# Kernel tuning notes

Measured on AMD Instinct MI355X. Metric: run time of the kernel, lower is better.

Reference implementation:

```python
import jax, jax.numpy as jnp
import numpy as np

VOCAB = 32000
EMB = 512
UNITS = 1024
B, T = 128, 256


def setup_inputs() -> dict:
    key = jax.random.key(0)
    ks = jax.random.split(key, 9)
    s = 0.05
    return {
        "tokens": jax.random.randint(ks[0], (B, T), 0, VOCAB),
        "emb_table": jax.random.normal(ks[1], (VOCAB, EMB), jnp.float32) * s,
        "Wx_f": jax.random.normal(ks[2], (EMB, 3 * UNITS), jnp.float32) * s,
        "Wh_f": jax.random.normal(ks[3], (UNITS, 3 * UNITS), jnp.float32) * s,
        "b_f": jnp.zeros((2, 3 * UNITS), jnp.float32),  # [input_bias, recurrent_bias] (reset_after=True)
        "Wx_b": jax.random.normal(ks[4], (EMB, 3 * UNITS), jnp.float32) * s,
        "Wh_b": jax.random.normal(ks[5], (UNITS, 3 * UNITS), jnp.float32) * s,
        "b_b": jnp.zeros((2, 3 * UNITS), jnp.float32),
        "fc_W": jax.random.normal(ks[6], (2 * UNITS, UNITS), jnp.float32) * s,
        "fc_b": jnp.zeros((UNITS,), jnp.float32),
    }


def _gru_dir(x_proj, mask, Wh, b_rec, reverse):
    # x_proj: [B,T,3U] precomputed input projections (z|r|h gate order, Keras),
    # mask: [B,T] bool. Keras GRU v2 semantics: reset_after=True,
    # sigmoid recurrent activation, tanh activation; masked steps carry state.
    b, u = x_proj.shape[0], Wh.shape[0]

    def step(h, inputs):
        xp, m = inputs  # [B,3U], [B]
        rec = h @ Wh + b_rec  # [B,3U]
        xz, xr, xh = jnp.split(xp, 3, axis=-1)
        rz, rr, rh = jnp.split(rec, 3, axis=-1)
        z = jax.nn.sigmoid(xz + rz)
        r = jax.nn.sigmoid(xr + rr)
        hh = jnp.tanh(xh + r * rh)
        h_new = z * h + (1.0 - z) * hh
        h_new = jnp.where(m[:, None], h_new, h)
        return h_new, h_new

    h0 = jnp.zeros((b, u), x_proj.dtype)
    xs = (jnp.swapaxes(x_proj, 0, 1), jnp.swapaxes(mask, 0, 1))  # time-major
    h_last, outs = jax.lax.scan(step, h0, xs, reverse=reverse)
    return jnp.swapaxes(outs, 0, 1), h_last  # [B,T,U], [B,U]


def reference(tokens, emb_table, Wx_f, Wh_f, b_f, Wx_b, Wh_b, b_b, fc_W, fc_b):
    mask = tokens != 0  # Embedding(mask_zero=True)
    x = emb_table[tokens]  # [B,T,E]
    xp_f = x @ Wx_f + b_f[0]
    xp_b = x @ Wx_b + b_b[0]
    out_f, h_f = _gru_dir(xp_f, mask, Wh_f, b_f[1], reverse=False)
    out_b, h_b = _gru_dir(xp_b, mask, Wh_b, b_b[1], reverse=True)
    output = jnp.concatenate([out_f, out_b], axis=-1)  # [B,T,2U]
    hidden = jnp.concatenate([h_f, h_b], axis=-1) @ fc_W + fc_b  # [B,U]
    return output, hidden
```

## Files before the change

kernel.cpp:

```cpp
#include <hip/hip_runtime.h>


#define T_SEQ 256
#define BATCH 128
#define EMB_D 512
#define UNITS 1024
#define NROWS (BATCH * T_SEQ)
#define N3U 3072
#define N6U 6144

typedef __attribute__((ext_vector_type(8))) __bf16 bfv8;
typedef __attribute__((ext_vector_type(4))) float f32x4;

__device__ inline unsigned short f2bf(float f) {
  union { float f; unsigned int u; } x; x.f = f;
  unsigned int u = x.u;
  unsigned int r = (u + 0x7fffu + ((u >> 16) & 1u)) >> 16;
  return (unsigned short)r;
}
__device__ inline float bf2f(unsigned short h) {
  union { unsigned int u; float f; } x; x.u = ((unsigned int)h) << 16;
  return x.f;
}
__device__ inline f32x4 mfma16(bfv8 a, bfv8 b, f32x4 c) {
  return __builtin_amdgcn_mfma_f32_16x16x32_bf16(a, b, c, 0, 0, 0);
}
__device__ inline void gl_lds16(const unsigned short* g, unsigned short* l) {
  __builtin_amdgcn_global_load_lds(
      (const __attribute__((address_space(1))) void*)g,
      (__attribute__((address_space(3))) void*)l, 16, 0, 0);
}

__global__ __launch_bounds__(256) void k_transpose(const float* __restrict__ src,
                                                   unsigned short* __restrict__ dst,
                                                   int K, int N) {
  __shared__ float tile[32][33];
  int k0 = blockIdx.x * 32, n0 = blockIdx.y * 32;
  int tx = threadIdx.x & 31, ty = threadIdx.x >> 5;
#pragma unroll
  for (int i = 0; i < 4; ++i)
    tile[ty + i * 8][tx] = src[(size_t)(k0 + ty + i * 8) * N + n0 + tx];
  __syncthreads();
#pragma unroll
  for (int i = 0; i < 4; ++i)
    dst[(size_t)(n0 + ty + i * 8) * K + k0 + tx] = f2bf(tile[tx][ty + i * 8]);
}

__global__ __launch_bounds__(256) void k_gather(const int* __restrict__ tokens,
                                                const float* __restrict__ emb,
                                                unsigned short* __restrict__ Xbf) {
  int idx = blockIdx.x * 256 + threadIdx.x;
  int row = idx >> 7;
  int c4 = (idx & 127) * 4;
  int tok = tokens[row];
  float4 v = *(const float4*)(emb + (size_t)tok * EMB_D + c4);
  ushort4 p;
  p.x = f2bf(v.x); p.y = f2bf(v.y); p.z = f2bf(v.z); p.w = f2bf(v.w);
  *(ushort4*)(Xbf + (size_t)row * EMB_D + c4) = p;
}

__global__ __launch_bounds__(256) void k_bias(const float* __restrict__ bf_,
                                              const float* __restrict__ bb_,
                                              float* __restrict__ biasX,
                                              float* __restrict__ biasH) {
  int i = blockIdx.x * 256 + threadIdx.x;
  if (i >= N6U) return;
  if (i < N3U) { biasX[i] = bf_[i];        biasH[i] = bf_[N3U + i]; }
  else         { biasX[i] = bb_[i - N3U];  biasH[i] = bb_[i]; }
}

__global__ __launch_bounds__(256) void k_gemm(const unsigned short* __restrict__ A,
                                              const unsigned short* __restrict__ BT,
                                              const float* __restrict__ bias,
                                              void* __restrict__ C,
                                              int M, int N, int K, int out_f32) {
  __shared__ unsigned short As[128 * 32];
  __shared__ unsigned short Bs[128 * 32];
  const int mt = blockIdx.x, nt = blockIdx.y;
  const int tid = threadIdx.x;
  const int wid = tid >> 6, lane = tid & 63;
  const int wm = (wid >> 1) * 64, wn = (wid & 1) * 64;
  const int l15 = lane & 15, lk = (lane >> 4) * 8;

  f32x4 acc[4][4];
#pragma unroll
  for (int i = 0; i < 4; ++i)
#pragma unroll
    for (int j = 0; j < 4; ++j) acc[i][j] = (f32x4){0.f, 0.f, 0.f, 0.f};

  const int r = tid >> 2;
  const int cc = (tid & 3) * 8;
  const unsigned short* ga0 = A + (size_t)(mt * 128 + r) * K + cc;
  const unsigned short* ga1 = ga0 + (size_t)64 * K;
  const unsigned short* gb0 = BT + (size_t)(nt * 128 + r) * K + cc;
  const unsigned short* gb1 = gb0 + (size_t)64 * K;
  unsigned short* lA0 = As + r * 32 + cc;
  unsigned short* lA1 = As + (64 + r) * 32 + cc;
  unsigned short* lB0 = Bs + r * 32 + cc;
  unsigned short* lB1 = Bs + (64 + r) * 32 + cc;

  for (int k0 = 0; k0 < K; k0 += 32) {
    __syncthreads();
    gl_lds16(ga0 + k0, lA0);
    gl_lds16(ga1 + k0, lA1);
    gl_lds16(gb0 + k0, lB0);
    gl_lds16(gb1 + k0, lB1);
    __syncthreads();
    bfv8 af[4], bfr[4];
#pragma unroll
    for (int i = 0; i < 4; ++i) {
      af[i]  = *(const bfv8*)(As + (wm + i * 16 + l15) * 32 + lk);
      bfr[i] = *(const bfv8*)(Bs + (wn + i * 16 + l15) * 32 + lk);
    }
#pragma unroll
    for (int i = 0; i < 4; ++i)
#pragma unroll
      for (int j = 0; j < 4; ++j) acc[i][j] = mfma16(af[i], bfr[j], acc[i][j]);
  }

#pragma unroll
  for (int j = 0; j < 4; ++j) {
    int col = nt * 128 + wn + j * 16 + l15;
    float bv = bias[col];
#pragma unroll
    for (int i = 0; i < 4; ++i) {
      int row0 = mt * 128 + wm + i * 16 + (lane >> 4) * 4;
#pragma unroll
      for (int q = 0; q < 4; ++q) {
        float v = acc[i][j][q] + bv;
        if (out_f32) ((float*)C)[(size_t)(row0 + q) * N + col] = v;
        else ((unsigned short*)C)[(size_t)(row0 + q) * N + col] = f2bf(v);
      }
    }
  }
}

__global__ __launch_bounds__(256) void k_scan(const unsigned short* __restrict__ XP,
                                              const unsigned short* __restrict__ WhT,
                                              const float* __restrict__ biasH,
                                              const int* __restrict__ tokens,
                                              unsigned short* __restrict__ hb0,
                                              unsigned short* __restrict__ hb1,
                                              float* __restrict__ out,
                                              unsigned int* __restrict__ bar) {
  __shared__ unsigned short Wl[3 * 128 * 16 * 8];
  __shared__ unsigned short bounce[64][16];
  const int bid = blockIdx.x;
  const int dir = bid >> 7;
  const int mg  = (bid >> 6) & 1;
  const int ut  = bid & 63;
  const int u0 = ut * 16, m0 = mg * 64;
  const int grp = bid >> 6;
  const int sub = bid & 7;

  for (int c = threadIdx.x; c < 6144; c += 256) {
    const int g  = c >> 11;
    const int kb = (c >> 4) & 127;
    const int uu = c & 15;
    *(uint4*)(Wl + (((g << 7) | kb) * 16 + uu) * 8) =
        *(const uint4*)(WhT + (((size_t)(dir * N3U + (g << 10) + u0 + uu)) << 10) + (kb << 3));
  }

  const int lane = threadIdx.x & 63, wid = threadIdx.x >> 6;
  const int l15 = lane & 15, hi = lane >> 4;
  const size_t aoff = ((size_t)(m0 + wid * 16 + l15) << 11) + (dir << 10) + (hi << 3);
  const int u = u0 + l15;
  const float bz  = biasH[dir * N3U + u];
  const float brg = biasH[dir * N3U + 1024 + u];
  const float bhg = biasH[dir * N3U + 2048 + u];
  const int ob = m0 + wid * 16 + (hi << 2);
  const int rb = wid * 16 + (hi << 2);
  const size_t woff = (dir << 10) + u;
  const int sr = threadIdx.x >> 2, sc4 = (threadIdx.x & 3) << 2;
  const size_t soff = ((size_t)(m0 + sr) << 11) + (dir << 10) + u0 + sc4;

  float hreg[4] = {0.f, 0.f, 0.f, 0.f};
  __syncthreads();

  for (int s = 0; s < T_SEQ; ++s) {
    const int t = dir ? (T_SEQ - 1 - s) : s;
    const unsigned short* hrd = (s & 1) ? hb0 : hb1;
    unsigned short* hwr       = (s & 1) ? hb1 : hb0;

    float xz[4], xr[4], xh[4]; int tok[4];
#pragma unroll
    for (int q = 0; q < 4; ++q) {
      const size_t xpo = ((size_t)((ob + q) * T_SEQ + t)) * N6U + dir * N3U + u;
      xz[q] = bf2f(XP[xpo]);
      xr[q] = bf2f(XP[xpo + 1024]);
      xh[q] = bf2f(XP[xpo + 2048]);
      tok[q] = tokens[(ob + q) * T_SEQ + t];
    }

    const unsigned short* ap = hrd + aoff;
    f32x4 az0 = {0.f,0.f,0.f,0.f}, az1 = az0, ar0 = az0, ar1 = az0, ah0 = az0, ah1 = az0;
#pragma unroll 4
    for (int ks = 0; ks < 16; ++ks) {
      bfv8 a0 = *(const bfv8*)(ap + (ks << 6));
      bfv8 a1 = *(const bfv8*)(ap + (ks << 6) + 32);
      const unsigned short* wp = Wl + (((ks << 3) + hi) * 16 + l15) * 8;
      bfv8 wz0 = *(const bfv8*)(wp);
      bfv8 wr0 = *(const bfv8*)(wp + (1 << 14));
      bfv8 wh0 = *(const bfv8*)(wp + (2 << 14));
      bfv8 wz1 = *(const bfv8*)(wp + 512);
      bfv8 wr1 = *(const bfv8*)(wp + (1 << 14) + 512);
      bfv8 wh1 = *(const bfv8*)(wp + (2 << 14) + 512);
      az0 = mfma16(a0, wz0, az0); ar0 = mfma16(a0, wr0, ar0); ah0 = mfma16(a0, wh0, ah0);
      az1 = mfma16(a1, wz1, az1); ar1 = mfma16(a1, wr1, ar1); ah1 = mfma16(a1, wh1, ah1);
    }
    f32x4 az = az0 + az1, ar = ar0 + ar1, ah = ah0 + ah1;

#pragma unroll
    for (int q = 0; q < 4; ++q) {
      const float z  = 1.f / (1.f + __expf(-(xz[q] + az[q] + bz)));
      const float r  = 1.f / (1.f + __expf(-(xr[q] + ar[q] + brg)));
      const float hh = tanhf(xh[q] + r * (ah[q] + bhg));
      float hn = z * hreg[q] + (1.f - z) * hh;
      if (tok[q] == 0) hn = hreg[q];
      hreg[q] = hn;
      bounce[rb + q][l15] = f2bf(hn);
      __builtin_nontemporal_store(hn, out + ((size_t)((ob + q) * T_SEQ + t) << 11) + woff);
    }

    __syncthreads();
    {
      unsigned long long v = *(const unsigned long long*)&bounce[sr][sc4];
      __hip_atomic_store((unsigned long long*)(hwr + soff), v,
                         __ATOMIC_RELAXED, __HIP_MEMORY_SCOPE_AGENT);
    }

    if (s + 1 < T_SEQ) {
      __syncthreads();
      if (threadIdx.x == 0)
        __hip_atomic_fetch_add(&bar[((grp << 3) | sub) << 6], 1u,
                               __ATOMIC_RELAXED, __HIP_MEMORY_SCOPE_AGENT);
      if (threadIdx.x < 8) {
        const unsigned tgt = 8u * (unsigned)(s + 1);
        unsigned int* p = &bar[((grp << 3) | (int)threadIdx.x) << 6];
        while (__hip_atomic_load(p, __ATOMIC_RELAXED, __HIP_MEMORY_SCOPE_AGENT) < tgt)
          __builtin_amdgcn_s_sleep(2);
        __builtin_amdgcn_fence(__ATOMIC_ACQUIRE, "agent");
      }
      __syncthreads();
    }
  }
}

extern "C" void kernel_launch(void* const* d_in, const int* in_sizes, int n_in,
                              void* d_out, int out_size, void* d_ws, size_t ws_size,
                              hipStream_t stream) {
  const int* tokens = (const int*)d_in[0];
  const float* emb  = (const float*)d_in[1];
  const float* Wx_f = (const float*)d_in[2];
  const float* Wh_f = (const float*)d_in[3];
  const float* b_f  = (const float*)d_in[4];
  const float* Wx_b = (const float*)d_in[5];
  const float* Wh_b = (const float*)d_in[6];
  const float* b_b  = (const float*)d_in[7];
  const float* fc_W = (const float*)d_in[8];
  const float* fc_b = (const float*)d_in[9];
  float* out = (float*)d_out;

  char* w = (char*)d_ws;
  unsigned short* XP  = (unsigned short*)w; w += (size_t)NROWS * N6U * 2;
  unsigned short* Xbf = (unsigned short*)w; w += (size_t)NROWS * EMB_D * 2;
  unsigned short* WxT = (unsigned short*)w; w += (size_t)N6U * EMB_D * 2;
  unsigned short* WhT = (unsigned short*)w; w += (size_t)N6U * UNITS * 2;
  unsigned short* fcWT = (unsigned short*)w; w += (size_t)UNITS * 2048 * 2;
  unsigned short* hb0 = (unsigned short*)w; w += (size_t)BATCH * 2048 * 2;
  unsigned short* hb1 = (unsigned short*)w; w += (size_t)BATCH * 2048 * 2;
  float* biasX = (float*)w; w += N6U * 4;
  float* biasH = (float*)w; w += N6U * 4;
  unsigned int* bar = (unsigned int*)w; w += 2048 * sizeof(unsigned int);

  (void)hipMemsetAsync((void*)hb0, 0, (size_t)BATCH * 2048 * 2 * 2, stream);
  (void)hipMemsetAsync((void*)bar, 0, 2048 * sizeof(unsigned int), stream);

  k_transpose<<<dim3(EMB_D / 32, N3U / 32), 256, 0, stream>>>(Wx_f, WxT, EMB_D, N3U);
  k_transpose<<<dim3(EMB_D / 32, N3U / 32), 256, 0, stream>>>(Wx_b, WxT + (size_t)N3U * EMB_D, EMB_D, N3U);
  k_transpose<<<dim3(UNITS / 32, N3U / 32), 256, 0, stream>>>(Wh_f, WhT, UNITS, N3U);
  k_transpose<<<dim3(UNITS / 32, N3U / 32), 256, 0, stream>>>(Wh_b, WhT + (size_t)N3U * UNITS, UNITS, N3U);
  k_transpose<<<dim3(2048 / 32, 1024 / 32), 256, 0, stream>>>(fc_W, fcWT, 2048, 1024);
  k_bias<<<24, 256, 0, stream>>>(b_f, b_b, biasX, biasH);
  k_gather<<<(NROWS * 128) / 256, 256, 0, stream>>>(tokens, emb, Xbf);

  k_gemm<<<dim3(NROWS / 128, N6U / 128), 256, 0, stream>>>(Xbf, WxT, biasX, XP, NROWS, N6U, EMB_D, 0);

  k_scan<<<256, 256, 0, stream>>>(XP, WhT, biasH, tokens, hb0, hb1, out, bar);

  k_gemm<<<dim3(1, 8), 256, 0, stream>>>(hb1, fcWT, fc_b, out + (size_t)NROWS * 2048, BATCH, UNITS, 2048, 1);
}
```

Measured before the change: 2.836 ms.

## Retile input projections time-major, prefetch per-step inputs, keep z/r weights in registers

The input-projection GEMM now writes its bf16 output in a time-major, per-block tiled layout, and tokens are transposed to time-major. This lets each scan block fetch a contiguous chunk for the next timestep into registers, overlapping the load with the current step's recurrent matmul, instead of issuing scattered global loads inside the serial loop. The z and r recurrent weight fragments are held in VGPRs, and only the h-gate weights stay in LDS, which cuts LDS traffic per step. The cost is heavy register pressure (64 bfv8 fragments plus prefetch buffers, hence the single-block launch bound) and scattered writes from the GEMM epilogue.

```diff
diff --git a/kernel.cpp b/kernel.cpp
--- a/kernel.cpp
+++ b/kernel.cpp
@@ -8,6 +8,7 @@
 #define NROWS (BATCH * T_SEQ)
 #define N3U 3072
 #define N6U 6144
+#define XT_STRIDE 786432
 
 typedef __attribute__((ext_vector_type(8))) __bf16 bfv8;
 typedef __attribute__((ext_vector_type(4))) float f32x4;
@@ -69,11 +70,18 @@
   else         { biasX[i] = bb_[i - N3U];  biasH[i] = bb_[i]; }
 }
 
+__global__ __launch_bounds__(256) void k_tokt(const int* __restrict__ tokens,
+                                              int* __restrict__ tokT) {
+  int i = blockIdx.x * 256 + threadIdx.x;
+  int b = i >> 8, t = i & 255;
+  tokT[t * BATCH + b] = tokens[i];
+}
+
 __global__ __launch_bounds__(256) void k_gemm(const unsigned short* __restrict__ A,
                                               const unsigned short* __restrict__ BT,
                                               const float* __restrict__ bias,
                                               void* __restrict__ C,
-                                              int M, int N, int K, int out_f32) {
+                                              int M, int N, int K, int mode) {
   __shared__ unsigned short As[128 * 32];
   __shared__ unsigned short Bs[128 * 32];
   const int mt = blockIdx.x, nt = blockIdx.y;
@@ -120,31 +128,45 @@
 
 #pragma unroll
   for (int j = 0; j < 4; ++j) {
-    int col = nt * 128 + wn + j * 16 + l15;
-    float bv = bias[col];
+    const int col = nt * 128 + wn + j * 16 + l15;
+    const float bv = bias[col];
+    const int dirc = (col >= N3U) ? 1 : 0;
+    const int cm = col - dirc * N3U;
+    const int g = cm >> 10;
+    const int uu = cm & 1023;
+    const size_t cbase = (size_t)dirc * 393216 + (size_t)(uu >> 4) * 6144 +
+                         (size_t)g * 16 + (uu & 15);
 #pragma unroll
     for (int i = 0; i < 4; ++i) {
-      int row0 = mt * 128 + wm + i * 16 + (lane >> 4) * 4;
+      const int row0 = mt * 128 + wm + i * 16 + (lane >> 4) * 4;
 #pragma unroll
       for (int q = 0; q < 4; ++q) {
-        float v = acc[i][j][q] + bv;
-        if (out_f32) ((float*)C)[(size_t)(row0 + q) * N + col] = v;
-        else ((unsigned short*)C)[(size_t)(row0 + q) * N + col] = f2bf(v);
+        const float v = acc[i][j][q] + bv;
+        const int row = row0 + q;
+        if (mode == 1) {
+          ((float*)C)[(size_t)row * N + col] = v;
+        } else {
+          const int b = row >> 8, tt = row & 255;
+          ((unsigned short*)C)[(size_t)tt * XT_STRIDE + cbase + (size_t)b * 48] = f2bf(v);
+        }
       }
     }
   }
 }
 
-__global__ __launch_bounds__(256) void k_scan(const unsigned short* __restrict__ XP,
-                                              const unsigned short* __restrict__ WhT,
-                                              const float* __restrict__ biasH,
-                                              const int* __restrict__ tokens,
-                                              unsigned short* __restrict__ hb0,
-                                              unsigned short* __restrict__ hb1,
-                                              float* __restrict__ out,
-                                              unsigned int* __restrict__ bar) {
-  __shared__ unsigned short Wl[3 * 128 * 16 * 8];
-  __shared__ unsigned short bounce[64][16];
+__global__ __launch_bounds__(256, 1) void k_scan(const unsigned short* __restrict__ XPn,
+                                                 const unsigned short* __restrict__ WhT,
+                                                 const float* __restrict__ biasH,
+                                                 const int* __restrict__ tokT,
+                                                 unsigned short* __restrict__ hb0,
+                                                 unsigned short* __restrict__ hb1,
+                                                 float* __restrict__ out,
+                                                 unsigned int* __restrict__ bar) {
+  __shared__ unsigned short Wl[128 * 16 * 8];
+  __shared__ unsigned short xb[64 * 48];
+  __shared__ int tkb[64];
+  __shared__ unsigned short bounce[64 * 24];
+
   const int bid = blockIdx.x;
   const int dir = bid >> 7;
   const int mg  = (bid >> 6) & 1;
@@ -152,27 +174,50 @@
   const int u0 = ut * 16, m0 = mg * 64;
   const int grp = bid >> 6;
   const int sub = bid & 7;
-
-  for (int c = threadIdx.x; c < 6144; c += 256) {
-    const int g  = c >> 11;
-    const int kb = (c >> 4) & 127;
-    const int uu = c & 15;
-    *(uint4*)(Wl + (((g << 7) | kb) * 16 + uu) * 8) =
-        *(const uint4*)(WhT + (((size_t)(dir * N3U + (g << 10) + u0 + uu)) << 10) + (kb << 3));
-  }
-
-  const int lane = threadIdx.x & 63, wid = threadIdx.x >> 6;
+  const int tid = threadIdx.x;
+
+  for (int c = tid; c < 2048; c += 256) {
+    const int kb = c >> 4, uu = c & 15;
+    *(uint4*)(Wl + c * 8) =
+        *(const uint4*)(WhT + (((size_t)(dir * N3U + 2048 + u0 + uu)) << 10) + (kb << 3));
+  }
+
+  const int lane = tid & 63, wid = tid >> 6;
   const int l15 = lane & 15, hi = lane >> 4;
+
+  bfv8 wza[16], wzb[16], wra[16], wrb[16];
+  {
+    const unsigned short* wgz = WhT + (((size_t)(dir * N3U + u0 + l15)) << 10);
+    const unsigned short* wgr = wgz + ((size_t)1024 << 10);
+#pragma unroll
+    for (int ks = 0; ks < 16; ++ks) {
+      wza[ks] = *(const bfv8*)(wgz + ((ks * 8 + hi) << 3));
+      wzb[ks] = *(const bfv8*)(wgz + ((ks * 8 + hi + 4) << 3));
+      wra[ks] = *(const bfv8*)(wgr + ((ks * 8 + hi) << 3));
+      wrb[ks] = *(const bfv8*)(wgr + ((ks * 8 + hi + 4) << 3));
+    }
+  }
+
   const size_t aoff = ((size_t)(m0 + wid * 16 + l15) << 11) + (dir << 10) + (hi << 3);
   const int u = u0 + l15;
   const float bz  = biasH[dir * N3U + u];
   const float brg = biasH[dir * N3U + 1024 + u];
   const float bhg = biasH[dir * N3U + 2048 + u];
-  const int ob = m0 + wid * 16 + (hi << 2);
   const int rb = wid * 16 + (hi << 2);
+  const int ob = m0 + rb;
   const size_t woff = (dir << 10) + u;
-  const int sr = threadIdx.x >> 2, sc4 = (threadIdx.x & 3) << 2;
+  const int sr = tid >> 2, sc4 = (tid & 3) << 2;
   const size_t soff = ((size_t)(m0 + sr) << 11) + (dir << 10) + u0 + sc4;
+
+  const unsigned short* xpb = XPn + (size_t)dir * 393216 + (size_t)ut * 6144 + (size_t)m0 * 48;
+
+  unsigned long long pf0, pf1, pf2; int pft = 0;
+  {
+    const int t0 = dir ? (T_SEQ - 1) : 0;
+    const unsigned long long* xs = (const unsigned long long*)(xpb + (size_t)t0 * XT_STRIDE);
+    pf0 = xs[tid]; pf1 = xs[tid + 256]; pf2 = xs[tid + 512];
+    if (tid < 64) pft = tokT[t0 * BATCH + m0 + tid];
+  }
 
   float hreg[4] = {0.f, 0.f, 0.f, 0.f};
   __syncthreads();
@@ -182,31 +227,41 @@
     const unsigned short* hrd = (s & 1) ? hb0 : hb1;
     unsigned short* hwr       = (s & 1) ? hb1 : hb0;
 
+    {
+      unsigned long long* xd = (unsigned long long*)xb;
+      xd[tid] = pf0; xd[tid + 256] = pf1; xd[tid + 512] = pf2;
+      if (tid < 64) tkb[tid] = pft;
+    }
+    __syncthreads();
+
     float xz[4], xr[4], xh[4]; int tok[4];
 #pragma unroll
     for (int q = 0; q < 4; ++q) {
-      const size_t xpo = ((size_t)((ob + q) * T_SEQ + t)) * N6U + dir * N3U + u;
-      xz[q] = bf2f(XP[xpo]);
-      xr[q] = bf2f(XP[xpo + 1024]);
-      xh[q] = bf2f(XP[xpo + 2048]);
-      tok[q] = tokens[(ob + q) * T_SEQ + t];
+      const int xo = (rb + q) * 48 + l15;
+      xz[q] = bf2f(xb[xo]);
+      xr[q] = bf2f(xb[xo + 16]);
+      xh[q] = bf2f(xb[xo + 32]);
+      tok[q] = tkb[rb + q];
+    }
+
+    if (s + 1 < T_SEQ) {
+      const int tn = dir ? (T_SEQ - 2 - s) : (s + 1);
+      const unsigned long long* xs = (const unsigned long long*)(xpb + (size_t)tn * XT_STRIDE);
+      pf0 = xs[tid]; pf1 = xs[tid + 256]; pf2 = xs[tid + 512];
+      if (tid < 64) pft = tokT[tn * BATCH + m0 + tid];
     }
 
     const unsigned short* ap = hrd + aoff;
     f32x4 az0 = {0.f,0.f,0.f,0.f}, az1 = az0, ar0 = az0, ar1 = az0, ah0 = az0, ah1 = az0;
-#pragma unroll 4
+#pragma unroll
     for (int ks = 0; ks < 16; ++ks) {
       bfv8 a0 = *(const bfv8*)(ap + (ks << 6));
       bfv8 a1 = *(const bfv8*)(ap + (ks << 6) + 32);
       const unsigned short* wp = Wl + (((ks << 3) + hi) * 16 + l15) * 8;
-      bfv8 wz0 = *(const bfv8*)(wp);
-      bfv8 wr0 = *(const bfv8*)(wp + (1 << 14));
-      bfv8 wh0 = *(const bfv8*)(wp + (2 << 14));
-      bfv8 wz1 = *(const bfv8*)(wp + 512);
-      bfv8 wr1 = *(const bfv8*)(wp + (1 << 14) + 512);
-      bfv8 wh1 = *(const bfv8*)(wp + (2 << 14) + 512);
-      az0 = mfma16(a0, wz0, az0); ar0 = mfma16(a0, wr0, ar0); ah0 = mfma16(a0, wh0, ah0);
-      az1 = mfma16(a1, wz1, az1); ar1 = mfma16(a1, wr1, ar1); ah1 = mfma16(a1, wh1, ah1);
+      bfv8 wh0 = *(const bfv8*)(wp);
+      bfv8 wh1 = *(const bfv8*)(wp + 512);
+      az0 = mfma16(a0, wza[ks], az0); ar0 = mfma16(a0, wra[ks], ar0); ah0 = mfma16(a0, wh0, ah0);
+      az1 = mfma16(a1, wzb[ks], az1); ar1 = mfma16(a1, wrb[ks], ar1); ah1 = mfma16(a1, wh1, ah1);
     }
     f32x4 az = az0 + az1, ar = ar0 + ar1, ah = ah0 + ah1;
 
@@ -218,25 +273,25 @@
       float hn = z * hreg[q] + (1.f - z) * hh;
       if (tok[q] == 0) hn = hreg[q];
       hreg[q] = hn;
-      bounce[rb + q][l15] = f2bf(hn);
+      bounce[(rb + q) * 24 + l15] = f2bf(hn);
       __builtin_nontemporal_store(hn, out + ((size_t)((ob + q) * T_SEQ + t) << 11) + woff);
     }
 
     __syncthreads();
     {
-      unsigned long long v = *(const unsigned long long*)&bounce[sr][sc4];
+      unsigned long long v = *(const unsigned long long*)(bounce + sr * 24 + sc4);
       __hip_atomic_store((unsigned long long*)(hwr + soff), v,
                          __ATOMIC_RELAXED, __HIP_MEMORY_SCOPE_AGENT);
     }
 
     if (s + 1 < T_SEQ) {
       __syncthreads();
-      if (threadIdx.x == 0)
+      if (tid == 0)
         __hip_atomic_fetch_add(&bar[((grp << 3) | sub) << 6], 1u,
                                __ATOMIC_RELAXED, __HIP_MEMORY_SCOPE_AGENT);
-      if (threadIdx.x < 8) {
+      if (tid < 8) {
         const unsigned tgt = 8u * (unsigned)(s + 1);
-        unsigned int* p = &bar[((grp << 3) | (int)threadIdx.x) << 6];
+        unsigned int* p = &bar[((grp << 3) | tid) << 6];
         while (__hip_atomic_load(p, __ATOMIC_RELAXED, __HIP_MEMORY_SCOPE_AGENT) < tgt)
           __builtin_amdgcn_s_sleep(2);
         __builtin_amdgcn_fence(__ATOMIC_ACQUIRE, "agent");
@@ -262,7 +317,7 @@
   float* out = (float*)d_out;
 
   char* w = (char*)d_ws;
-  unsigned short* XP  = (unsigned short*)w; w += (size_t)NROWS * N6U * 2;
+  unsigned short* XPn = (unsigned short*)w; w += (size_t)NROWS * N6U * 2;
   unsigned short* Xbf = (unsigned short*)w; w += (size_t)NROWS * EMB_D * 2;
   unsigned short* WxT = (unsigned short*)w; w += (size_t)N6U * EMB_D * 2;
   unsigned short* WhT = (unsigned short*)w; w += (size_t)N6U * UNITS * 2;
@@ -271,6 +326,7 @@
   unsigned short* hb1 = (unsigned short*)w; w += (size_t)BATCH * 2048 * 2;
   float* biasX = (float*)w; w += N6U * 4;
   float* biasH = (float*)w; w += N6U * 4;
+  int* tokT = (int*)w; w += NROWS * 4;
   unsigned int* bar = (unsigned int*)w; w += 2048 * sizeof(unsigned int);
 
   (void)hipMemsetAsync((void*)hb0, 0, (size_t)BATCH * 2048 * 2 * 2, stream);
@@ -282,11 +338,12 @@
   k_transpose<<<dim3(UNITS / 32, N3U / 32), 256, 0, stream>>>(Wh_b, WhT + (size_t)N3U * UNITS, UNITS, N3U);
   k_transpose<<<dim3(2048 / 32, 1024 / 32), 256, 0, stream>>>(fc_W, fcWT, 2048, 1024);
   k_bias<<<24, 256, 0, stream>>>(b_f, b_b, biasX, biasH);
+  k_tokt<<<NROWS / 256, 256, 0, stream>>>(tokens, tokT);
   k_gather<<<(NROWS * 128) / 256, 256, 0, stream>>>(tokens, emb, Xbf);
 
-  k_gemm<<<dim3(NROWS / 128, N6U / 128), 256, 0, stream>>>(Xbf, WxT, biasX, XP, NROWS, N6U, EMB_D, 0);
-
-  k_scan<<<256, 256, 0, stream>>>(XP, WhT, biasH, tokens, hb0, hb1, out, bar);
+  k_gemm<<<dim3(NROWS / 128, N6U / 128), 256, 0, stream>>>(Xbf, WxT, biasX, XPn, NROWS, N6U, EMB_D, 0);
+
+  k_scan<<<256, 256, 0, stream>>>(XPn, WhT, biasH, tokT, hb0, hb1, out, bar);
 
   k_gemm<<<dim3(1, 8), 256, 0, stream>>>(hb1, fcWT, fc_b, out + (size_t)NROWS * 2048, BATCH, UNITS, 2048, 1);
 }
```

Result: slower. 3.211 ms (+13.2%).
